# Kernel optimization log

Measured on AMD Instinct MI355X. Metric: run time of the kernel, lower is better.

## Reference

```python
import jax, jax.numpy as jnp
import numpy as np

EPS = 1e-5
SCALE = 4


def _conv(x, w, b=None, stride=1, pad=0):
    y = jax.lax.conv_general_dilated(
        x, w, (stride, stride), ((pad, pad), (pad, pad)),
        dimension_numbers=("NCHW", "OIHW", "NCHW"))
    if b is not None:
        y = y + b[None, :, None, None]
    return y


def _bn(x, g, b, m, v):
    # inference-mode BatchNorm2d with running stats
    scale = g / jnp.sqrt(v + EPS)
    return (x - m[None, :, None, None]) * scale[None, :, None, None] + b[None, :, None, None]


def setup_inputs() -> dict:
    key = jax.random.key(0)
    ks = jax.random.split(key, 20)
    B, H, W = 2, 112, 256
    d = {}
    d["patch"] = jax.random.normal(ks[0], (B, 3, SCALE * H, SCALE * W), jnp.float32)
    d["disp"] = jax.random.normal(ks[1], (B, 1, H, W), jnp.float32)
    # encode: conv(3->256, k=s=4, no bias) + BN + ReLU + conv(256->256, k3 p1, no bias) + BN + ReLU
    d["w_enc1"] = jax.random.normal(ks[2], (256, 3, SCALE, SCALE), jnp.float32) * 0.05
    d["bn1_g"] = jax.random.uniform(ks[3], (256,), jnp.float32) + 0.5
    d["bn1_b"] = jax.random.normal(ks[4], (256,), jnp.float32) * 0.01
    d["bn1_m"] = jax.random.normal(ks[5], (256,), jnp.float32) * 0.01
    d["bn1_v"] = jax.random.uniform(ks[6], (256,), jnp.float32) + 0.5
    d["w_enc2"] = jax.random.normal(ks[7], (256, 256, 3, 3), jnp.float32) * 0.02
    d["bn2_g"] = jax.random.uniform(ks[8], (256,), jnp.float32) + 0.5
    d["bn2_b"] = jax.random.normal(ks[9], (256,), jnp.float32) * 0.01
    d["bn2_m"] = jax.random.normal(ks[10], (256,), jnp.float32) * 0.01
    d["bn2_v"] = jax.random.uniform(ks[11], (256,), jnp.float32) + 0.5
    # conv_disp_feat: conv(257->256, k3 p1) + ReLU + conv(256->512, k3 p1) + ReLU + conv(512->144, k1)
    d["w_c1"] = jax.random.normal(ks[12], (256, 257, 3, 3), jnp.float32) * 0.02
    d["b_c1"] = jax.random.normal(ks[13], (256,), jnp.float32) * 0.01
    d["w_c2"] = jax.random.normal(ks[14], (512, 256, 3, 3), jnp.float32) * 0.02
    d["b_c2"] = jax.random.normal(ks[15], (512,), jnp.float32) * 0.01
    d["w_c3"] = jax.random.normal(ks[16], (SCALE * SCALE * 9, 512, 1, 1), jnp.float32) * 0.02
    d["b_c3"] = jax.random.normal(ks[17], (SCALE * SCALE * 9,), jnp.float32) * 0.01
    return d


def reference(patch, disp, w_enc1, bn1_g, bn1_b, bn1_m, bn1_v,
              w_enc2, bn2_g, bn2_b, bn2_m, bn2_v,
              w_c1, b_c1, w_c2, b_c2, w_c3, b_c3):
    B, _, H, W = disp.shape
    # encoder
    feat = jax.nn.relu(_bn(_conv(patch, w_enc1, stride=SCALE), bn1_g, bn1_b, bn1_m, bn1_v))
    feat = jax.nn.relu(_bn(_conv(feat, w_enc2, pad=1), bn2_g, bn2_b, bn2_m, bn2_v))
    # mask prediction
    x = jnp.concatenate([disp, feat], axis=1)  # (B, 257, H, W)
    x = jax.nn.relu(_conv(x, w_c1, b_c1, pad=1))
    x = jax.nn.relu(_conv(x, w_c2, b_c2, pad=1))
    raw_mask = _conv(x, w_c3, b_c3)  # (B, 144, H, W)
    mask = raw_mask.reshape(B, 1, 9, SCALE, SCALE, H, W)
    mask = jax.nn.softmax(mask, axis=2)
    # F.unfold(disp, k=3, p=1): gather 3x3 neighborhoods, order (ky, kx)
    padd = jnp.pad(disp, ((0, 0), (0, 0), (1, 1), (1, 1)))
    neigh = jnp.stack([padd[:, :, ky:ky + H, kx:kx + W]
                       for ky in range(3) for kx in range(3)], axis=2)  # (B,1,9,H,W)
    up = (mask * neigh[:, :, :, None, None, :, :]).sum(axis=2)  # (B,1,s,s,H,W)
    up = up.transpose(0, 1, 4, 2, 5, 3).reshape(B, 1, SCALE * H, SCALE * W)
    return up
```

## Files before the change

kernel.cpp:

```cpp
#include <hip/hip_runtime.h>
#include <hip/hip_bf16.h>

constexpr int B_ = 2;
constexpr int H_ = 112;
constexpr int W_ = 256;
constexpr int HW_ = H_ * W_;
constexpr int PH_ = 448;
constexpr int PW_ = 1024;
constexpr float EPS_ = 1e-5f;

typedef __bf16 bf16x8 __attribute__((ext_vector_type(8)));
typedef float f32x4 __attribute__((ext_vector_type(4)));

__device__ __forceinline__ bf16x8 ld_bf16x8(const __hip_bfloat16* p) {
    return *reinterpret_cast<const bf16x8*>(p);
}
__device__ __forceinline__ bf16x8 zero_bf16x8() {
    union { int4 i; bf16x8 v; } u;
    u.i = make_int4(0, 0, 0, 0);
    return u.v;
}
__device__ __forceinline__ void gload_lds16(const __hip_bfloat16* g, __hip_bfloat16* lds) {
    __builtin_amdgcn_global_load_lds(
        (const __attribute__((address_space(1))) void*)g,
        (__attribute__((address_space(3))) void*)lds, 16, 0, 0);
}

__global__ void prep_w3_pack(const float* __restrict__ w, int COUT, int CSRC, int COFF,
                             const float* __restrict__ g, const float* __restrict__ vvar,
                             __hip_bfloat16* __restrict__ dst) {
    int idx = blockIdx.x * 256 + threadIdx.x;
    int CF = COUT / 16;
    int n = 9 * 8 * CF * 512;
    if (idx >= n) return;
    int j = idx & 7;
    int lane = (idx >> 3) & 63;
    int rest = idx >> 9;
    int cf = rest % CF;
    int rest2 = rest / CF;
    int ks = rest2 & 7;
    int tap = rest2 >> 3;
    int cout = cf * 16 + (lane & 15);
    int ci = ks * 32 + (lane >> 4) * 8 + j;
    float sc = g ? g[cout] * rsqrtf(vvar[cout] + EPS_) : 1.f;
    dst[idx] = __float2bfloat16(w[((size_t)cout * CSRC + ci + COFF) * 9 + tap] * sc);
}

__global__ void prep_c3_pack(const float* __restrict__ w, __hip_bfloat16* __restrict__ dst) {
    int idx = blockIdx.x * 256 + threadIdx.x;
    if (idx >= 16 * 9 * 512) return;
    int j = idx & 7;
    int lane = (idx >> 3) & 63;
    int rest = idx >> 9;
    int mf = rest % 9;
    int ks = rest / 9;
    int row = mf * 16 + (lane & 15);
    int ci = ks * 32 + (lane >> 4) * 8 + j;
    dst[idx] = __float2bfloat16(w[(size_t)row * 512 + ci]);
}

__global__ void prep_misc_kernel(const float* __restrict__ w_c1,
                                 const float* __restrict__ g, const float* __restrict__ bb,
                                 const float* __restrict__ m, const float* __restrict__ v,
                                 float* __restrict__ wd_c1, float* __restrict__ bias2) {
    int idx = blockIdx.x * 256 + threadIdx.x;
    if (idx < 256 * 9) {
        int co = idx / 9, tap = idx % 9;
        wd_c1[idx] = w_c1[(size_t)co * 257 * 9 + tap];
    } else if (idx < 256 * 9 + 256) {
        int co = idx - 256 * 9;
        float sc = g[co] * rsqrtf(v[co] + EPS_);
        bias2[co] = bb[co] - m[co] * sc;
    }
}

__global__ __launch_bounds__(256) void enc1_nhwc_kernel(
    const float* __restrict__ patch, const float* __restrict__ wgt,
    const float* __restrict__ g, const float* __restrict__ bb,
    const float* __restrict__ m, const float* __restrict__ v,
    __hip_bfloat16* __restrict__ out) {
    const int tid = threadIdx.x;
    const int px = tid & 63;
    const int wid = tid >> 6;
    const int bx = blockIdx.x;
    const int w0 = (bx & 3) * 64;
    const int h = bx >> 2;
    const int b = blockIdx.z;
    const int w = w0 + px;

    float p[3][4][4];
#pragma unroll
    for (int c = 0; c < 3; ++c)
#pragma unroll
        for (int ky = 0; ky < 4; ++ky) {
            float4 f = *reinterpret_cast<const float4*>(
                patch + (((size_t)b * 3 + c) * PH_ + 4 * h + ky) * PW_ + 4 * w);
            p[c][ky][0] = f.x; p[c][ky][1] = f.y; p[c][ky][2] = f.z; p[c][ky][3] = f.w;
        }

    __shared__ __hip_bfloat16 s[64][258];

    const int kbase = __builtin_amdgcn_readfirstlane(wid * 64);
    for (int i = 0; i < 64; ++i) {
        int k = kbase + i;
        const float* wk = wgt + (size_t)k * 48;
        float acc = 0.f;
#pragma unroll
        for (int c = 0; c < 3; ++c)
#pragma unroll
            for (int ky = 0; ky < 4; ++ky)
#pragma unroll
                for (int kx = 0; kx < 4; ++kx)
                    acc += p[c][ky][kx] * wk[(c * 4 + ky) * 4 + kx];
        float sc = g[k] * rsqrtf(v[k] + EPS_);
        float o = fmaxf(acc * sc + (bb[k] - m[k] * sc), 0.f);
        s[px][k] = __float2bfloat16(o);
    }
    __syncthreads();
    const size_t base = (((size_t)b * H_ + h) * W_ + w0) * 256;
    for (int j = tid; j < 64 * 128; j += 256) {
        int elem = j * 2;
        int pp = elem >> 8;
        int k = elem & 255;
        unsigned int val = *reinterpret_cast<const unsigned int*>(&s[pp][k]);
        *reinterpret_cast<unsigned int*>(out + base + elem) = val;
    }
}

template <int COUT, bool HAS_DISP>
__global__ __launch_bounds__(256) void conv3x3_mfma2(
    const __hip_bfloat16* __restrict__ in,
    const __hip_bfloat16* __restrict__ wPack,
    const float* __restrict__ bias,
    const float* __restrict__ disp,
    const float* __restrict__ wd,
    __hip_bfloat16* __restrict__ out) {
    constexpr int CIN = 256;
    constexpr int CF = COUT / 16;
    const int tid = threadIdx.x;
    const int lane = tid & 63;
    const int wid = tid >> 6;
    const int wm = wid & 1;
    const int wn = wid >> 1;
    const int lr = lane & 15;
    const int lg = lane >> 4;

    const int bx = blockIdx.x;
    const int w0 = (bx & 1) * 128;
    const int h = bx >> 1;
    const int coutBase = blockIdx.y * 128;
    const int b = blockIdx.z;

    const int coutW = coutBase + wm * 64;
    const int cfW = coutW >> 4;
    const int pxW = wn * 64;

    __shared__ __hip_bfloat16 sIn[2][3][130][32];

    f32x4 acc[4][4] = {};

    const __hip_bfloat16* inb = in + (size_t)b * HW_ * CIN;
    const __hip_bfloat16* wBase = wPack + (size_t)cfW * 512 + (size_t)lane * 8;

    auto STAGE = [&](int buf, int c0) {
#pragma unroll
        for (int i = 0; i < 6; ++i) {
            const int idx = wid * 6 + i;
            const int row = idx >> 3, grp = idx & 7;
            const int y = h + row - 1;
            __hip_bfloat16* ldsb = &sIn[buf][row][1 + grp * 16][0];
            if ((unsigned)y < (unsigned)H_) {
                const __hip_bfloat16* gp = inb +
                    ((size_t)y * W_ + w0 + grp * 16 + (lane >> 2)) * CIN + c0 + (lane & 3) * 8;
                gload_lds16(gp, ldsb);
            } else {
                *reinterpret_cast<int4*>(reinterpret_cast<char*>(ldsb) + lane * 16) =
                    make_int4(0, 0, 0, 0);
            }
        }
        if (tid < 24) {
            const int row = tid >> 3, p2 = (tid >> 2) & 1, sub = tid & 3;
            const int pxl = p2 ? 129 : 0;
            const int y = h + row - 1, x = w0 + pxl - 1;
            bf16x8 v = zero_bf16x8();
            if ((unsigned)y < (unsigned)H_ && (unsigned)x < (unsigned)W_)
                v = ld_bf16x8(inb + ((size_t)y * W_ + x) * CIN + c0 + sub * 8);
            *reinterpret_cast<bf16x8*>(&sIn[buf][row][pxl][sub * 8]) = v;
        }
    };

    STAGE(0, 0);
    __syncthreads();
    int cur = 0;
    for (int ks = 0; ks < 8; ++ks) {
        if (ks < 7) STAGE(cur ^ 1, (ks + 1) * 32);
#pragma unroll
        for (int tap = 0; tap < 9; ++tap) {
            const int ky = tap / 3, kx = tap % 3;
            bf16x8 a[4];
#pragma unroll
            for (int mf = 0; mf < 4; ++mf)
                a[mf] = ld_bf16x8(wBase + ((size_t)(tap * 8 + ks) * CF + mf) * 512);
#pragma unroll
            for (int nf = 0; nf < 4; ++nf) {
                bf16x8 bv = *reinterpret_cast<const bf16x8*>(
                    &sIn[cur][ky][pxW + nf * 16 + lr + kx][lg * 8]);
#pragma unroll
                for (int mf = 0; mf < 4; ++mf)
                    acc[mf][nf] = __builtin_amdgcn_mfma_f32_16x16x32_bf16(
                        a[mf], bv, acc[mf][nf], 0, 0, 0);
            }
        }
        __syncthreads();
        cur ^= 1;
    }

    const size_t rowBase = ((size_t)b * H_ + h) * W_;
#pragma unroll
    for (int nf = 0; nf < 4; ++nf) {
        const int px = w0 + pxW + nf * 16 + lr;
        float dnb[9];
        if (HAS_DISP) {
#pragma unroll
            for (int t = 0; t < 9; ++t) {
                int yy = h + t / 3 - 1, xx = px + t % 3 - 1;
                dnb[t] = ((unsigned)yy < (unsigned)H_ && (unsigned)xx < (unsigned)W_)
                             ? disp[((size_t)b * H_ + yy) * W_ + xx]
                             : 0.f;
            }
        }
#pragma unroll
        for (int mf = 0; mf < 4; ++mf) {
            alignas(8) __hip_bfloat16 ov[4];
#pragma unroll
            for (int r = 0; r < 4; ++r) {
                const int cout = coutW + mf * 16 + lg * 4 + r;
                float o = acc[mf][nf][r] + bias[cout];
                if (HAS_DISP) {
                    float s = 0.f;
#pragma unroll
                    for (int t = 0; t < 9; ++t) s += wd[cout * 9 + t] * dnb[t];
                    o += s;
                }
                ov[r] = __float2bfloat16(fmaxf(o, 0.f));
            }
            *reinterpret_cast<uint2*>(out + (rowBase + px) * COUT + coutW + mf * 16 + lg * 4) =
                *reinterpret_cast<const uint2*>(ov);
        }
    }
}

__global__ __launch_bounds__(256) void c3_fused_kernel(
    const __hip_bfloat16* __restrict__ x2,
    const __hip_bfloat16* __restrict__ wPack,
    const float* __restrict__ bias,
    const float* __restrict__ disp,
    float* __restrict__ outp) {
    const int tid = threadIdx.x;
    const int lane = tid & 63;
    const int wid = tid >> 6;
    const int lr = lane & 15;
    const int lg = lane >> 4;
    const int bx = blockIdx.x;
    const int w0 = (bx & 3) * 64;
    const int h = bx >> 2;
    const int b = blockIdx.z;
    const int pxw = w0 + wid * 16 + lr;

    f32x4 acc[9] = {};
    const __hip_bfloat16* inp = x2 + (((size_t)b * H_ + h) * W_ + pxw) * 512;
    const __hip_bfloat16* wl = wPack + (size_t)lane * 8;
#pragma unroll 4
    for (int ks = 0; ks < 16; ++ks) {
        const int c0 = ks * 32 + lg * 8;
        bf16x8 bv = ld_bf16x8(inp + c0);
#pragma unroll
        for (int mf = 0; mf < 9; ++mf) {
            bf16x8 av = ld_bf16x8(wl + ((size_t)ks * 9 + mf) * 512);
            acc[mf] = __builtin_amdgcn_mfma_f32_16x16x32_bf16(av, bv, acc[mf], 0, 0, 0);
        }
    }

    float dnb[9];
#pragma unroll
    for (int t = 0; t < 9; ++t) {
        int yy = h + t / 3 - 1, xx = pxw + t % 3 - 1;
        dnb[t] = ((unsigned)yy < (unsigned)H_ && (unsigned)xx < (unsigned)W_)
                     ? disp[((size_t)b * H_ + yy) * W_ + xx]
                     : 0.f;
    }
    float oo[4];
#pragma unroll
    for (int r = 0; r < 4; ++r) {
        const int st = lg * 4 + r;
        float sv[9], mx = -1e30f;
#pragma unroll
        for (int mf = 0; mf < 9; ++mf) {
            sv[mf] = acc[mf][r] + bias[mf * 16 + st];
            mx = fmaxf(mx, sv[mf]);
        }
        float sum = 0.f, wsum = 0.f;
#pragma unroll
        for (int mf = 0; mf < 9; ++mf) {
            float e = __expf(sv[mf] - mx);
            sum += e;
            wsum += e * dnb[mf];
        }
        oo[r] = wsum / sum;
    }
    float4 o4 = make_float4(oo[0], oo[1], oo[2], oo[3]);
    *reinterpret_cast<float4*>(outp + ((size_t)b * PH_ + 4 * h + lg) * PW_ + 4 * pxw) = o4;
}

extern "C" void kernel_launch(void* const* d_in, const int* in_sizes, int n_in,
                              void* d_out, int out_size, void* d_ws, size_t ws_size,
                              hipStream_t stream) {
    const float* patch = (const float*)d_in[0];
    const float* disp = (const float*)d_in[1];
    const float* w_enc1 = (const float*)d_in[2];
    const float* bn1_g = (const float*)d_in[3];
    const float* bn1_b = (const float*)d_in[4];
    const float* bn1_m = (const float*)d_in[5];
    const float* bn1_v = (const float*)d_in[6];
    const float* w_enc2 = (const float*)d_in[7];
    const float* bn2_g = (const float*)d_in[8];
    const float* bn2_b = (const float*)d_in[9];
    const float* bn2_m = (const float*)d_in[10];
    const float* bn2_v = (const float*)d_in[11];
    const float* w_c1 = (const float*)d_in[12];
    const float* b_c1 = (const float*)d_in[13];
    const float* w_c2 = (const float*)d_in[14];
    const float* b_c2 = (const float*)d_in[15];
    const float* w_c3 = (const float*)d_in[16];
    const float* b_c3 = (const float*)d_in[17];
    float* out = (float*)d_out;

    char* ws = (char*)d_ws;
    const size_t S1 = (size_t)B_ * HW_ * 256 * sizeof(__hip_bfloat16);
    const size_t S2 = (size_t)B_ * HW_ * 512 * sizeof(__hip_bfloat16);
    __hip_bfloat16* feat1 = (__hip_bfloat16*)ws;   ws += S1;
    __hip_bfloat16* feat2 = (__hip_bfloat16*)ws;   ws += S1;
    __hip_bfloat16* x1    = (__hip_bfloat16*)ws;   ws += S1;
    __hip_bfloat16* x2    = (__hip_bfloat16*)ws;   ws += S2;
    __hip_bfloat16* wP_enc2 = (__hip_bfloat16*)ws; ws += (size_t)9 * 256 * 256 * 2;
    __hip_bfloat16* wP_c1   = (__hip_bfloat16*)ws; ws += (size_t)9 * 256 * 256 * 2;
    __hip_bfloat16* wP_c2   = (__hip_bfloat16*)ws; ws += (size_t)9 * 512 * 256 * 2;
    __hip_bfloat16* wP_c3   = (__hip_bfloat16*)ws; ws += (size_t)16 * 9 * 512 * 2;
    float* bias2 = (float*)ws;                     ws += 256 * 4;
    float* wd_c1 = (float*)ws;                     ws += 256 * 9 * 4;

    dim3 blk(256, 1, 1);

    prep_w3_pack<<<dim3((9 * 256 * 256 + 255) / 256), blk, 0, stream>>>(
        w_enc2, 256, 256, 0, bn2_g, bn2_v, wP_enc2);
    prep_w3_pack<<<dim3((9 * 256 * 256 + 255) / 256), blk, 0, stream>>>(
        w_c1, 256, 257, 1, nullptr, nullptr, wP_c1);
    prep_w3_pack<<<dim3((9 * 512 * 256 + 255) / 256), blk, 0, stream>>>(
        w_c2, 512, 256, 0, nullptr, nullptr, wP_c2);
    prep_c3_pack<<<dim3((16 * 9 * 512 + 255) / 256), blk, 0, stream>>>(w_c3, wP_c3);
    prep_misc_kernel<<<dim3((256 * 9 + 256 + 255) / 256), blk, 0, stream>>>(
        w_c1, bn2_g, bn2_b, bn2_m, bn2_v, wd_c1, bias2);

    enc1_nhwc_kernel<<<dim3(H_ * 4, 1, B_), blk, 0, stream>>>(
        patch, w_enc1, bn1_g, bn1_b, bn1_m, bn1_v, feat1);
    conv3x3_mfma2<256, false><<<dim3(2 * H_, 2, B_), blk, 0, stream>>>(
        feat1, wP_enc2, bias2, nullptr, nullptr, feat2);
    conv3x3_mfma2<256, true><<<dim3(2 * H_, 2, B_), blk, 0, stream>>>(
        feat2, wP_c1, b_c1, disp, wd_c1, x1);
    conv3x3_mfma2<512, false><<<dim3(2 * H_, 4, B_), blk, 0, stream>>>(
        x1, wP_c2, b_c2, nullptr, nullptr, x2);
    c3_fused_kernel<<<dim3(H_ * 4, 1, B_), blk, 0, stream>>>(
        x2, wP_c3, b_c3, disp, out);
}
```

Measured before the change: 400.8 us.

## Retile conv3x3 MFMA kernel to 256 couts x 64 pixels with 64-channel stages

```diff
diff --git a/kernel.cpp b/kernel.cpp
--- a/kernel.cpp
+++ b/kernel.cpp
@@ -128,7 +128,7 @@
 }
 
 template <int COUT, bool HAS_DISP>
-__global__ __launch_bounds__(256) void conv3x3_mfma2(
+__global__ __launch_bounds__(256, 3) void conv3x3_mfma3(
     const __hip_bfloat16* __restrict__ in,
     const __hip_bfloat16* __restrict__ wPack,
     const float* __restrict__ bias,
@@ -146,18 +146,18 @@
     const int lg = lane >> 4;
 
     const int bx = blockIdx.x;
-    const int w0 = (bx & 1) * 128;
-    const int h = bx >> 1;
-    const int coutBase = blockIdx.y * 128;
+    const int w0 = (bx & 3) * 64;
+    const int h = bx >> 2;
+    const int coutBase = blockIdx.y * 256;
     const int b = blockIdx.z;
 
-    const int coutW = coutBase + wm * 64;
+    const int coutW = coutBase + wm * 128;
     const int cfW = coutW >> 4;
-    const int pxW = wn * 64;
-
-    __shared__ __hip_bfloat16 sIn[2][3][130][32];
-
-    f32x4 acc[4][4] = {};
+    const int pxW = wn * 32;
+
+    __shared__ __hip_bfloat16 sIn[2][3][2][66][32];
+
+    f32x4 acc[8][2] = {};
 
     const __hip_bfloat16* inb = in + (size_t)b * HW_ * CIN;
     const __hip_bfloat16* wBase = wPack + (size_t)cfW * 512 + (size_t)lane * 8;
@@ -166,49 +166,61 @@
 #pragma unroll
         for (int i = 0; i < 6; ++i) {
             const int idx = wid * 6 + i;
-            const int row = idx >> 3, grp = idx & 7;
+            const int row = idx >> 3;
+            const int rem = idx & 7;
+            const int ks2 = rem >> 2;
+            const int grp = rem & 3;
             const int y = h + row - 1;
-            __hip_bfloat16* ldsb = &sIn[buf][row][1 + grp * 16][0];
+            __hip_bfloat16* ldsb = &sIn[buf][row][ks2][1 + grp * 16][0];
             if ((unsigned)y < (unsigned)H_) {
                 const __hip_bfloat16* gp = inb +
-                    ((size_t)y * W_ + w0 + grp * 16 + (lane >> 2)) * CIN + c0 + (lane & 3) * 8;
+                    ((size_t)y * W_ + w0 + grp * 16 + (lane >> 2)) * CIN +
+                    c0 + ks2 * 32 + (lane & 3) * 8;
                 gload_lds16(gp, ldsb);
             } else {
                 *reinterpret_cast<int4*>(reinterpret_cast<char*>(ldsb) + lane * 16) =
                     make_int4(0, 0, 0, 0);
             }
         }
-        if (tid < 24) {
-            const int row = tid >> 3, p2 = (tid >> 2) & 1, sub = tid & 3;
-            const int pxl = p2 ? 129 : 0;
+        if (tid < 48) {
+            const int row = tid >> 4;
+            const int rem = tid & 15;
+            const int ks2 = rem >> 3;
+            const int sub = rem & 7;
+            const int pxl = (sub >> 2) ? 65 : 0;
+            const int cp = sub & 3;
             const int y = h + row - 1, x = w0 + pxl - 1;
             bf16x8 v = zero_bf16x8();
             if ((unsigned)y < (unsigned)H_ && (unsigned)x < (unsigned)W_)
-                v = ld_bf16x8(inb + ((size_t)y * W_ + x) * CIN + c0 + sub * 8);
-            *reinterpret_cast<bf16x8*>(&sIn[buf][row][pxl][sub * 8]) = v;
+                v = ld_bf16x8(inb + ((size_t)y * W_ + x) * CIN + c0 + ks2 * 32 + cp * 8);
+            *reinterpret_cast<bf16x8*>(&sIn[buf][row][ks2][pxl][cp * 8]) = v;
         }
     };
 
     STAGE(0, 0);
     __syncthreads();
     int cur = 0;
-    for (int ks = 0; ks < 8; ++ks) {
-        if (ks < 7) STAGE(cur ^ 1, (ks + 1) * 32);
+    for (int c = 0; c < 4; ++c) {
+        if (c < 3) STAGE(cur ^ 1, (c + 1) * 64);
 #pragma unroll
         for (int tap = 0; tap < 9; ++tap) {
             const int ky = tap / 3, kx = tap % 3;
-            bf16x8 a[4];
-#pragma unroll
-            for (int mf = 0; mf < 4; ++mf)
-                a[mf] = ld_bf16x8(wBase + ((size_t)(tap * 8 + ks) * CF + mf) * 512);
-#pragma unroll
-            for (int nf = 0; nf < 4; ++nf) {
-                bf16x8 bv = *reinterpret_cast<const bf16x8*>(
-                    &sIn[cur][ky][pxW + nf * 16 + lr + kx][lg * 8]);
-#pragma unroll
-                for (int mf = 0; mf < 4; ++mf)
-                    acc[mf][nf] = __builtin_amdgcn_mfma_f32_16x16x32_bf16(
-                        a[mf], bv, acc[mf][nf], 0, 0, 0);
+#pragma unroll
+            for (int ks2 = 0; ks2 < 2; ++ks2) {
+                const int ks = c * 2 + ks2;
+                bf16x8 a[8];
+#pragma unroll
+                for (int mf = 0; mf < 8; ++mf)
+                    a[mf] = ld_bf16x8(wBase + ((size_t)(tap * 8 + ks) * CF + mf) * 512);
+#pragma unroll
+                for (int nf = 0; nf < 2; ++nf) {
+                    bf16x8 bv = *reinterpret_cast<const bf16x8*>(
+                        &sIn[cur][ky][ks2][pxW + nf * 16 + lr + kx][lg * 8]);
+#pragma unroll
+                    for (int mf = 0; mf < 8; ++mf)
+                        acc[mf][nf] = __builtin_amdgcn_mfma_f32_16x16x32_bf16(
+                            a[mf], bv, acc[mf][nf], 0, 0, 0);
+                }
             }
         }
         __syncthreads();
@@ -217,7 +229,7 @@
 
     const size_t rowBase = ((size_t)b * H_ + h) * W_;
 #pragma unroll
-    for (int nf = 0; nf < 4; ++nf) {
+    for (int nf = 0; nf < 2; ++nf) {
         const int px = w0 + pxW + nf * 16 + lr;
         float dnb[9];
         if (HAS_DISP) {
@@ -230,7 +242,7 @@
             }
         }
 #pragma unroll
-        for (int mf = 0; mf < 4; ++mf) {
+        for (int mf = 0; mf < 8; ++mf) {
             alignas(8) __hip_bfloat16 ov[4];
 #pragma unroll
             for (int r = 0; r < 4; ++r) {
@@ -363,11 +375,11 @@
 
     enc1_nhwc_kernel<<<dim3(H_ * 4, 1, B_), blk, 0, stream>>>(
         patch, w_enc1, bn1_g, bn1_b, bn1_m, bn1_v, feat1);
-    conv3x3_mfma2<256, false><<<dim3(2 * H_, 2, B_), blk, 0, stream>>>(
+    conv3x3_mfma3<256, false><<<dim3(H_ * 4, 1, B_), blk, 0, stream>>>(
         feat1, wP_enc2, bias2, nullptr, nullptr, feat2);
-    conv3x3_mfma2<256, true><<<dim3(2 * H_, 2, B_), blk, 0, stream>>>(
+    conv3x3_mfma3<256, true><<<dim3(H_ * 4, 1, B_), blk, 0, stream>>>(
         feat2, wP_c1, b_c1, disp, wd_c1, x1);
-    conv3x3_mfma2<512, false><<<dim3(2 * H_, 4, B_), blk, 0, stream>>>(
+    conv3x3_mfma3<512, false><<<dim3(H_ * 4, 2, B_), blk, 0, stream>>>(
         x1, wP_c2, b_c2, nullptr, nullptr, x2);
     c3_fused_kernel<<<dim3(H_ * 4, 1, B_), blk, 0, stream>>>(
         x2, wP_c3, b_c3, disp, out);
```

New measurement: 485.9 us. +21.2%, slower.
